# Kernel optimization log

Measured on AMD Instinct MI355X. Metric: run time of the kernel, lower is better.

## Reference

```python
import jax, jax.numpy as jnp
import numpy as np

N_NODES = 50000
N_EDGES = 1600000
HIDDEN = 64
N_BLOCKS = 2
N_ITERS = 2


def setup_inputs() -> dict:
    key = jax.random.key(0)
    ks = jax.random.split(key, 10)
    hidden = jax.random.normal(ks[0], (N_NODES, HIDDEN), dtype=jnp.float32)
    src = jax.random.randint(ks[1], (N_EDGES,), 0, N_NODES)
    dst = jax.random.randint(ks[2], (N_EDGES,), 0, N_NODES)
    s = 0.05  # keep MLP activations well-scaled
    W1 = jax.random.normal(ks[3], (N_BLOCKS, 3 * HIDDEN, 128), dtype=jnp.float32) * s
    b1 = jax.random.normal(ks[4], (N_BLOCKS, 128), dtype=jnp.float32) * s
    W2 = jax.random.normal(ks[5], (N_BLOCKS, 128, 128), dtype=jnp.float32) * s
    b2 = jax.random.normal(ks[6], (N_BLOCKS, 128), dtype=jnp.float32) * s
    W3 = jax.random.normal(ks[7], (N_BLOCKS, 128, HIDDEN), dtype=jnp.float32) * s
    b3 = jax.random.normal(ks[8], (N_BLOCKS, HIDDEN), dtype=jnp.float32) * s
    return {"hidden": hidden, "src": src, "dst": dst,
            "W1": W1, "b1": b1, "W2": W2, "b2": b2, "W3": W3, "b3": b3}


def _node_update(hidden, src, dst, w1, c1, w2, c2, w3, c3):
    # global rep: sum of all node hidden reps, broadcast to every node
    grep = jnp.broadcast_to(jnp.sum(hidden, axis=0, keepdims=True), hidden.shape)
    # mailbox sum: gather src features, segment-sum into dst
    msgs = hidden[src]                                  # [E, H]
    agg = jax.ops.segment_sum(msgs, dst, num_segments=hidden.shape[0])  # [N, H]
    x = jnp.concatenate([agg, hidden, grep], axis=1)    # [N, 3H]
    h = jax.nn.relu(x @ w1 + c1)
    h = jax.nn.relu(h @ w2 + c2)
    out = h @ w3 + c3
    # row-wise L2 (fro over dim=1) normalization
    norm = jnp.sqrt(jnp.sum(out * out, axis=1, keepdims=True))
    return out / norm


def reference(hidden, src, dst, W1, b1, W2, b2, W3, b3):
    for blk in range(N_BLOCKS):
        for _ in range(N_ITERS):
            hidden = _node_update(hidden, src, dst,
                                  W1[blk], b1[blk], W2[blk], b2[blk], W3[blk], b3[blk])
    return hidden
```

## Files before the change

kernel.cpp:

```cpp
#include <hip/hip_runtime.h>
#include <math.h>

#define NN 50000
#define NE 1600000
#define H  64

#define SHIFT 7
#define NPBKT 128
#define NB    391
#define CHUNK 4096
#define NCH   391

typedef __attribute__((ext_vector_type(8))) short s16v8;
typedef __attribute__((ext_vector_type(4))) float f32v4;
typedef __attribute__((ext_vector_type(8))) _Float16 f16v8;
typedef unsigned short u16;
typedef unsigned int   u32;

__device__ __forceinline__ u16 f2bf(float x) {
    union { float f; unsigned u; } v; v.f = x;
    unsigned r = v.u + 0x7FFF + ((v.u >> 16) & 1);
    return (u16)(r >> 16);
}
__device__ __forceinline__ float bf2f(u16 h) {
    union { float f; unsigned u; } v; v.u = ((unsigned)h) << 16; return v.f;
}

__global__ __launch_bounds__(256) void hist_kernel(const int* __restrict__ dst,
                                                   int* __restrict__ chunkhist) {
    __shared__ int h[NB];
    const int c = blockIdx.x;
    for (int b = threadIdx.x; b < NB; b += 256) h[b] = 0;
    __syncthreads();
    const int e0 = c * CHUNK, e1 = min(NE, e0 + CHUNK);
    for (int e = e0 + threadIdx.x; e < e1; e += 256)
        atomicAdd(&h[dst[e] >> SHIFT], 1);
    __syncthreads();
    for (int b = threadIdx.x; b < NB; b += 256)
        chunkhist[c * NB + b] = h[b];
}

__global__ __launch_bounds__(512) void cscan_kernel(int* __restrict__ chunkhist,
                                                    int* __restrict__ bbase) {
    __shared__ int s[512];
    const int t = threadIdx.x;
    int tot = 0;
    if (t < NB)
        for (int c = 0; c < NCH; ++c) tot += chunkhist[c * NB + t];
    s[t] = (t < NB) ? tot : 0;
    __syncthreads();
    for (int d = 1; d < 512; d <<= 1) {
        int v = (t >= d) ? s[t - d] : 0;
        __syncthreads();
        s[t] += v;
        __syncthreads();
    }
    if (t < NB) {
        int base = s[t] - tot;
        bbase[t] = base;
        if (t == NB - 1) bbase[NB] = s[t];
        int run = base;
        for (int c = 0; c < NCH; ++c) {
            int tmp = chunkhist[c * NB + t];
            chunkhist[c * NB + t] = run;
            run += tmp;
        }
    }
}

__global__ __launch_bounds__(256) void scat_kernel(const int* __restrict__ src,
                                                   const int* __restrict__ dst,
                                                   const int* __restrict__ chunkhist,
                                                   u32* __restrict__ bin) {
    __shared__ int base[NB];
    __shared__ int cur[NB];
    const int c = blockIdx.x;
    for (int b = threadIdx.x; b < NB; b += 256) {
        base[b] = chunkhist[c * NB + b];
        cur[b] = 0;
    }
    __syncthreads();
    const int e0 = c * CHUNK, e1 = min(NE, e0 + CHUNK);
    for (int e = e0 + threadIdx.x; e < e1; e += 256) {
        int d = dst[e];
        int b = d >> SHIFT;
        int p = atomicAdd(&cur[b], 1);
        bin[base[b] + p] = (u32)src[e] | ((u32)(d & (NPBKT - 1)) << 16);
    }
}

__global__ __launch_bounds__(256) void binB_kernel(const u32* __restrict__ bin,
                                                   const int* __restrict__ bbase,
                                                   int* __restrict__ off,
                                                   u16* __restrict__ csr) {
    __shared__ int deg[NPBKT];
    __shared__ int sc[NPBKT];
    __shared__ int cur[NPBKT];
    const int b = blockIdx.x, t = threadIdx.x;
    const int seg0 = bbase[b], seg1 = bbase[b + 1];
    if (t < NPBKT) { deg[t] = 0; cur[t] = 0; }
    __syncthreads();
    for (int i = seg0 + t; i < seg1; i += 256)
        atomicAdd(&deg[(bin[i] >> 16) & (NPBKT - 1)], 1);
    __syncthreads();
    if (t < NPBKT) sc[t] = deg[t];
    __syncthreads();
    for (int d = 1; d < NPBKT; d <<= 1) {
        int v = 0;
        if (t < NPBKT && t >= d) v = sc[t - d];
        __syncthreads();
        if (t < NPBKT) sc[t] += v;
        __syncthreads();
    }
    if (t < NPBKT) {
        sc[t] -= deg[t];
        int node = b * NPBKT + t;
        if (node < NN) off[node] = seg0 + sc[t];
        if (b == 0 && t == 0) off[NN] = NE;
    }
    __syncthreads();
    for (int i = seg0 + t; i < seg1; i += 256) {
        u32 e = bin[i];
        int n = (e >> 16) & (NPBKT - 1);
        int p = atomicAdd(&cur[n], 1);
        csr[seg0 + sc[n] + p] = (u16)(e & 0xFFFF);
    }
}

__global__ __launch_bounds__(256) void prep_kernel(const float* __restrict__ W1,
        const float* __restrict__ W2, const float* __restrict__ W3,
        u16* __restrict__ wt) {
    int idx = blockIdx.x * 256 + threadIdx.x;
    if (idx >= 2 * 40960) return;
    int b = idx / 40960, r = idx - b * 40960;
    float v; int hioff, losz;
    if (r < 16384) {
        int col = r >> 7, k = r & 127;
        v = W1[b * 24576 + k * 128 + col];
        hioff = b * 81920 + r; losz = 16384;
    } else if (r < 32768) {
        int rr = r - 16384; int col = rr >> 7, k = rr & 127;
        v = W2[b * 16384 + k * 128 + col];
        hioff = b * 81920 + 32768 + rr; losz = 16384;
    } else {
        int rr = r - 32768; int col = rr >> 7, k = rr & 127;
        v = W3[b * 8192 + k * 64 + col];
        hioff = b * 81920 + 65536 + rr; losz = 8192;
    }
    u16 hi = f2bf(v);
    u16 lo = f2bf(v - bf2f(hi));
    wt[hioff] = hi; wt[hioff + losz] = lo;
}

__global__ __launch_bounds__(256) void grep_kernel(const float* __restrict__ h,
                                                   float* __restrict__ partial,
                                                   _Float16* __restrict__ h16) {
    const int c  = threadIdx.x & 63;
    const int rl = threadIdx.x >> 6;
    float acc = 0.f;
    for (int r = blockIdx.x * 4 + rl; r < NN; r += gridDim.x * 4) {
        float v = h[r * H + c];
        h16[r * H + c] = (_Float16)v;
        acc += v;
    }
    __shared__ float s[4][64];
    s[rl][c] = acc;
    __syncthreads();
    if (threadIdx.x < 64)
        partial[blockIdx.x * 64 + threadIdx.x] =
            s[0][threadIdx.x] + s[1][threadIdx.x] +
            s[2][threadIdx.x] + s[3][threadIdx.x];
}

__global__ __launch_bounds__(1024) void b1e_kernel(const float* __restrict__ partial,
        int nparts,
        const float* __restrict__ W1, const float* __restrict__ b1,
        float* __restrict__ b1e) {
    __shared__ float sg[16][64];
    __shared__ float g[64];
    const int t = threadIdx.x;
    const int c = t & 63, rl = t >> 6;
    float s = 0.f;
    for (int i = rl; i < nparts; i += 16) s += partial[i * 64 + c];
    sg[rl][c] = s;
    __syncthreads();
    if (t < 64) {
        float a = 0.f;
#pragma unroll
        for (int j = 0; j < 16; ++j) a += sg[j][t];
        g[t] = a;
    }
    __syncthreads();
    if (t < 128) {
        float s2 = b1[t];
        for (int k = 0; k < 64; ++k)
            s2 = fmaf(g[k], W1[(128 + k) * 128 + t], s2);
        b1e[t] = s2;
    }
}

#define MLP_MFMA(d, a, b) d = __builtin_amdgcn_mfma_f32_16x16x32_bf16(a, b, d, 0, 0, 0)

__global__ __launch_bounds__(512, 4) void fused_mlp(
    const _Float16* __restrict__ h16in, const float* __restrict__ hin,
    const float* __restrict__ b1e, const u16* __restrict__ wt,
    const float* __restrict__ b2, const float* __restrict__ b3,
    const u16* __restrict__ csr, const int* __restrict__ off,
    float* __restrict__ out, _Float16* __restrict__ h16out,
    float* __restrict__ colpart)
{
    __shared__ u16 hhi[64 * 128], hlo[64 * 128];
    __shared__ float ssw[4][64];
    __shared__ float colp[64];
    const int t = threadIdx.x;
    const int wl = t >> 6, lane = t & 63;
    const int li = lane & 15, g = lane >> 4;
    const int n0 = blockIdx.x * 64;

    const u16* w1hi = wt;
    const u16* w1lo = wt + 16384;
    const u16* w2hi = wt + 32768;
    const u16* w2lo = wt + 49152;
    const u16* w3hi = wt + 65536;
    const u16* w3lo = wt + 73728;

    {
        const int nl = lane >> 3, sub = lane & 7;
        const int node = min(n0 + wl * 8 + nl, NN - 1);
        const int beg = off[node], end = off[node + 1];
        float a[8] = {0.f, 0.f, 0.f, 0.f, 0.f, 0.f, 0.f, 0.f};
        int e = beg;
        for (; e + 1 < end; e += 2) {
            const int s0 = csr[e], s1 = csr[e + 1];
            f16v8 v0 = *(const f16v8*)&h16in[(size_t)s0 * 64 + sub * 8];
            f16v8 v1 = *(const f16v8*)&h16in[(size_t)s1 * 64 + sub * 8];
#pragma unroll
            for (int j = 0; j < 8; ++j) a[j] += (float)v0[j] + (float)v1[j];
        }
        if (e < end) {
            const int s0 = csr[e];
            f16v8 v0 = *(const f16v8*)&h16in[(size_t)s0 * 64 + sub * 8];
#pragma unroll
            for (int j = 0; j < 8; ++j) a[j] += (float)v0[j];
        }
        const int row = wl * 8 + nl;
        s16v8 hv, lv;
#pragma unroll
        for (int j = 0; j < 8; ++j) {
            u16 hb = f2bf(a[j]);
            hv[j] = (short)hb;
            lv[j] = (short)f2bf(a[j] - bf2f(hb));
        }
        const int addr = row * 128 + ((sub ^ (row & 7)) << 3);
        *(s16v8*)&hhi[addr] = hv;
        *(s16v8*)&hlo[addr] = lv;
    }
    {
        const int row = t >> 3, c8 = t & 7;
        const int node = min(n0 + row, NN - 1);
        const float* sp = hin + (size_t)node * 64 + c8 * 8;
        float4 u0 = *(const float4*)sp;
        float4 u1 = *(const float4*)(sp + 4);
        float f[8] = {u0.x, u0.y, u0.z, u0.w, u1.x, u1.y, u1.z, u1.w};
        s16v8 hv, lv;
#pragma unroll
        for (int j = 0; j < 8; ++j) {
            u16 hb = f2bf(f[j]);
            hv[j] = (short)hb;
            lv[j] = (short)f2bf(f[j] - bf2f(hb));
        }
        const int cb = 8 + c8;
        const int addr = row * 128 + ((cb ^ (row & 7)) << 3);
        *(s16v8*)&hhi[addr] = hv;
        *(s16v8*)&hlo[addr] = lv;
    }
    __syncthreads();

    {
        const int col = wl * 16 + li;
        s16v8 Bh[4], Bl[4];
#pragma unroll
        for (int ks = 0; ks < 4; ++ks) {
            Bh[ks] = *(const s16v8*)(w1hi + col * 128 + ks * 32 + g * 8);
            Bl[ks] = *(const s16v8*)(w1lo + col * 128 + ks * 32 + g * 8);
        }
        f32v4 acc[4];
#pragma unroll
        for (int i = 0; i < 4; ++i) acc[i] = (f32v4){0.f, 0.f, 0.f, 0.f};
#pragma unroll
        for (int rt = 0; rt < 4; ++rt) {
            const int row = rt * 16 + li;
#pragma unroll
            for (int ks = 0; ks < 4; ++ks) {
                const int kb = ks * 4 + g;
                const int addr = row * 128 + ((kb ^ (row & 7)) << 3);
                s16v8 Ah = *(const s16v8*)&hhi[addr];
                s16v8 Al = *(const s16v8*)&hlo[addr];
                MLP_MFMA(acc[rt], Ah, Bh[ks]);
                MLP_MFMA(acc[rt], Ah, Bl[ks]);
                MLP_MFMA(acc[rt], Al, Bh[ks]);
            }
        }
        __syncthreads();
        const float bb = b1e[col];
        const int cb = col >> 3, c7 = col & 7;
#pragma unroll
        for (int rt = 0; rt < 4; ++rt) {
#pragma unroll
            for (int r = 0; r < 4; ++r) {
                float hv = fmaxf(acc[rt][r] + bb, 0.f);
                u16 hb = f2bf(hv);
                u16 lb = f2bf(hv - bf2f(hb));
                const int row = rt * 16 + g * 4 + r;
                const int addr = row * 128 + (((cb ^ (row & 7)) << 3) | c7);
                hhi[addr] = hb; hlo[addr] = lb;
            }
        }
    }
    __syncthreads();

    {
        const int col = wl * 16 + li;
        s16v8 Bh[4], Bl[4];
#pragma unroll
        for (int ks = 0; ks < 4; ++ks) {
            Bh[ks] = *(const s16v8*)(w2hi + col * 128 + ks * 32 + g * 8);
            Bl[ks] = *(const s16v8*)(w2lo + col * 128 + ks * 32 + g * 8);
        }
        f32v4 acc[4];
#pragma unroll
        for (int i = 0; i < 4; ++i) acc[i] = (f32v4){0.f, 0.f, 0.f, 0.f};
#pragma unroll
        for (int rt = 0; rt < 4; ++rt) {
            const int row = rt * 16 + li;
#pragma unroll
            for (int ks = 0; ks < 4; ++ks) {
                const int kb = ks * 4 + g;
                const int addr = row * 128 + ((kb ^ (row & 7)) << 3);
                s16v8 Ah = *(const s16v8*)&hhi[addr];
                s16v8 Al = *(const s16v8*)&hlo[addr];
                MLP_MFMA(acc[rt], Ah, Bh[ks]);
                MLP_MFMA(acc[rt], Ah, Bl[ks]);
                MLP_MFMA(acc[rt], Al, Bh[ks]);
            }
        }
        __syncthreads();
        const float bb = b2[col];
        const int cb = col >> 3, c7 = col & 7;
#pragma unroll
        for (int rt = 0; rt < 4; ++rt) {
#pragma unroll
            for (int r = 0; r < 4; ++r) {
                float hv = fmaxf(acc[rt][r] + bb, 0.f);
                u16 hb = f2bf(hv);
                u16 lb = f2bf(hv - bf2f(hb));
                const int row = rt * 16 + g * 4 + r;
                const int addr = row * 128 + (((cb ^ (row & 7)) << 3) | c7);
                hhi[addr] = hb; hlo[addr] = lb;
            }
        }
    }
    __syncthreads();

    float v[4][4];
    if (wl < 4) {
        const int col = wl * 16 + li;
        s16v8 Bh[4], Bl[4];
#pragma unroll
        for (int ks = 0; ks < 4; ++ks) {
            Bh[ks] = *(const s16v8*)(w3hi + col * 128 + ks * 32 + g * 8);
            Bl[ks] = *(const s16v8*)(w3lo + col * 128 + ks * 32 + g * 8);
        }
        f32v4 acc[4];
#pragma unroll
        for (int i = 0; i < 4; ++i) acc[i] = (f32v4){0.f, 0.f, 0.f, 0.f};
#pragma unroll
        for (int rt = 0; rt < 4; ++rt) {
            const int row = rt * 16 + li;
#pragma unroll
            for (int ks = 0; ks < 4; ++ks) {
                const int kb = ks * 4 + g;
                const int addr = row * 128 + ((kb ^ (row & 7)) << 3);
                s16v8 Ah = *(const s16v8*)&hhi[addr];
                s16v8 Al = *(const s16v8*)&hlo[addr];
                MLP_MFMA(acc[rt], Ah, Bh[ks]);
                MLP_MFMA(acc[rt], Ah, Bl[ks]);
                MLP_MFMA(acc[rt], Al, Bh[ks]);
            }
        }
        const float bb = b3[col];
#pragma unroll
        for (int rt = 0; rt < 4; ++rt) {
#pragma unroll
            for (int r = 0; r < 4; ++r) {
                float vv = acc[rt][r] + bb;
                v[rt][r] = vv;
                float s2 = vv * vv;
#pragma unroll
                for (int o = 1; o <= 8; o <<= 1) s2 += __shfl_xor(s2, o);
                if (li == 0) ssw[wl][rt * 16 + g * 4 + r] = s2;
            }
        }
    }
    __syncthreads();
    if (wl < 4) {
        const int col = wl * 16 + li;
        float cs = 0.f;
#pragma unroll
        for (int rt = 0; rt < 4; ++rt) {
#pragma unroll
            for (int r = 0; r < 4; ++r) {
                const int row = rt * 16 + g * 4 + r;
                const float tot = ssw[0][row] + ssw[1][row] +
                                  ssw[2][row] + ssw[3][row];
                const float inv = rsqrtf(tot);
                const int node = n0 + row;
                float ov = v[rt][r] * inv;
                if (node < NN) {
                    out[(size_t)node * 64 + col] = ov;
                    h16out[(size_t)node * 64 + col] = (_Float16)ov;
                    cs += ov;
                }
            }
        }
        cs += __shfl_xor(cs, 16);
        cs += __shfl_xor(cs, 32);
        if (g == 0) colp[col] = cs;
    }
    __syncthreads();
    if (t < 64)
        colpart[(size_t)blockIdx.x * 64 + t] = colp[t];
}

extern "C" void kernel_launch(void* const* d_in, const int* in_sizes, int n_in,
                              void* d_out, int out_size, void* d_ws, size_t ws_size,
                              hipStream_t stream) {
    const float* hidden = (const float*)d_in[0];
    const int*   src    = (const int*)d_in[1];
    const int*   dst    = (const int*)d_in[2];
    const float* W1f    = (const float*)d_in[3];
    const float* b1f    = (const float*)d_in[4];
    const float* W2f    = (const float*)d_in[5];
    const float* b2f    = (const float*)d_in[6];
    const float* W3f    = (const float*)d_in[7];
    const float* b3f    = (const float*)d_in[8];

    const int NBLK = (NN + 63) / 64;

    float* b1e     = (float*)d_ws;
    float* partA   = b1e + 128;
    float* partB   = partA + 256 * 64;
    float* hA      = partB + (size_t)NBLK * 64;
    int*   bbase   = (int*)(hA + (size_t)NN * H);
    int*   off     = bbase + (NB + 1);
    int*   chist   = off + (NN + 1);
    u32*   bin     = (u32*)(chist + NCH * NB);
    u16*   csr     = (u16*)(bin + NE);
    u16*   wt      = (u16*)(((uintptr_t)(csr + NE) + 255) & ~(uintptr_t)255);
    _Float16* h16a = (_Float16*)(wt + 2 * 81920);
    _Float16* h16b = h16a + (size_t)NN * H;

    hist_kernel<<<NCH, 256, 0, stream>>>(dst, chist);
    cscan_kernel<<<1, 512, 0, stream>>>(chist, bbase);
    scat_kernel<<<NCH, 256, 0, stream>>>(src, dst, chist, bin);
    binB_kernel<<<NB, 256, 0, stream>>>(bin, bbase, off, csr);
    prep_kernel<<<(2 * 40960 + 255) / 256, 256, 0, stream>>>(W1f, W2f, W3f, wt);

    grep_kernel<<<256, 256, 0, stream>>>(hidden, partA, h16a);

    const float* hin = hidden;
    float* houts[4] = { hA, (float*)d_out, hA, (float*)d_out };
    _Float16* h16bufs[2] = { h16a, h16b };

    for (int it = 0; it < 4; ++it) {
        const int blk = it >> 1;
        const float* part = (it == 0) ? partA : partB;
        const int nparts  = (it == 0) ? 256 : NBLK;
        b1e_kernel<<<1, 1024, 0, stream>>>(part, nparts,
            W1f + blk * 24576, b1f + blk * 128, b1e);
        fused_mlp<<<NBLK, 512, 0, stream>>>(
            h16bufs[it & 1], hin, b1e, wt + blk * 81920,
            b2f + blk * 128, b3f + blk * 64, csr, off,
            houts[it], h16bufs[(it + 1) & 1], partB);
        hin = houts[it];
    }
}
```

Measured before the change: 409.5 us.

## Fuse global-sum bias reduction into MLP kernel and unroll edge gather

Removes the separate single-block b1e kernel by having every fused_mlp block reduce the per-block column partials and compute the effective first-layer bias itself. Partial-sum buffers are ping-ponged so blocks can read the previous iteration's partials while writing new ones. The edge gather loop is unrolled to four edges and the self-feature load is issued earlier to overlap latency. This trades four small serial launches for redundant per-block reduction work over all partials.

```diff
diff --git a/kernel.cpp b/kernel.cpp
--- a/kernel.cpp
+++ b/kernel.cpp
@@ -172,38 +172,13 @@
             s[2][threadIdx.x] + s[3][threadIdx.x];
 }
 
-__global__ __launch_bounds__(1024) void b1e_kernel(const float* __restrict__ partial,
-        int nparts,
-        const float* __restrict__ W1, const float* __restrict__ b1,
-        float* __restrict__ b1e) {
-    __shared__ float sg[16][64];
-    __shared__ float g[64];
-    const int t = threadIdx.x;
-    const int c = t & 63, rl = t >> 6;
-    float s = 0.f;
-    for (int i = rl; i < nparts; i += 16) s += partial[i * 64 + c];
-    sg[rl][c] = s;
-    __syncthreads();
-    if (t < 64) {
-        float a = 0.f;
-#pragma unroll
-        for (int j = 0; j < 16; ++j) a += sg[j][t];
-        g[t] = a;
-    }
-    __syncthreads();
-    if (t < 128) {
-        float s2 = b1[t];
-        for (int k = 0; k < 64; ++k)
-            s2 = fmaf(g[k], W1[(128 + k) * 128 + t], s2);
-        b1e[t] = s2;
-    }
-}
-
 #define MLP_MFMA(d, a, b) d = __builtin_amdgcn_mfma_f32_16x16x32_bf16(a, b, d, 0, 0, 0)
 
 __global__ __launch_bounds__(512, 4) void fused_mlp(
     const _Float16* __restrict__ h16in, const float* __restrict__ hin,
-    const float* __restrict__ b1e, const u16* __restrict__ wt,
+    const float* __restrict__ part, int nparts,
+    const float* __restrict__ W1g, const float* __restrict__ b1,
+    const u16* __restrict__ wt,
     const float* __restrict__ b2, const float* __restrict__ b3,
     const u16* __restrict__ csr, const int* __restrict__ off,
     float* __restrict__ out, _Float16* __restrict__ h16out,
@@ -212,6 +187,8 @@
     __shared__ u16 hhi[64 * 128], hlo[64 * 128];
     __shared__ float ssw[4][64];
     __shared__ float colp[64];
+    __shared__ float gg[64];
+    __shared__ float b1eL[128];
     const int t = threadIdx.x;
     const int wl = t >> 6, lane = t & 63;
     const int li = lane & 15, g = lane >> 4;
@@ -225,54 +202,84 @@
     const u16* w3lo = wt + 73728;
 
     {
+        float* sgf = (float*)hhi;
+        const int c = t & 63, rl = t >> 6;
+        float s = 0.f;
+        for (int i = rl; i < nparts; i += 8) s += part[i * 64 + c];
+        sgf[rl * 64 + c] = s;
+        __syncthreads();
+        if (t < 64) {
+            float a = 0.f;
+#pragma unroll
+            for (int j = 0; j < 8; ++j) a += sgf[j * 64 + t];
+            gg[t] = a;
+        }
+        __syncthreads();
+        if (t < 128) {
+            float s2 = b1[t];
+            for (int k = 0; k < 64; ++k)
+                s2 = fmaf(gg[k], W1g[(128 + k) * 128 + t], s2);
+            b1eL[t] = s2;
+        }
+    }
+
+    {
+        const int row = t >> 3, c8 = t & 7;
+        const int hnode = min(n0 + row, NN - 1);
+        const float* sp = hin + (size_t)hnode * 64 + c8 * 8;
+        float4 u0 = *(const float4*)sp;
+        float4 u1 = *(const float4*)(sp + 4);
+
         const int nl = lane >> 3, sub = lane & 7;
         const int node = min(n0 + wl * 8 + nl, NN - 1);
         const int beg = off[node], end = off[node + 1];
         float a[8] = {0.f, 0.f, 0.f, 0.f, 0.f, 0.f, 0.f, 0.f};
         int e = beg;
-        for (; e + 1 < end; e += 2) {
-            const int s0 = csr[e], s1 = csr[e + 1];
+        for (; e + 3 < end; e += 4) {
+            const int s0 = csr[e],     s1 = csr[e + 1];
+            const int s2 = csr[e + 2], s3 = csr[e + 3];
             f16v8 v0 = *(const f16v8*)&h16in[(size_t)s0 * 64 + sub * 8];
             f16v8 v1 = *(const f16v8*)&h16in[(size_t)s1 * 64 + sub * 8];
-#pragma unroll
-            for (int j = 0; j < 8; ++j) a[j] += (float)v0[j] + (float)v1[j];
-        }
-        if (e < end) {
+            f16v8 v2 = *(const f16v8*)&h16in[(size_t)s2 * 64 + sub * 8];
+            f16v8 v3 = *(const f16v8*)&h16in[(size_t)s3 * 64 + sub * 8];
+#pragma unroll
+            for (int j = 0; j < 8; ++j)
+                a[j] += ((float)v0[j] + (float)v1[j]) +
+                        ((float)v2[j] + (float)v3[j]);
+        }
+        for (; e < end; ++e) {
             const int s0 = csr[e];
             f16v8 v0 = *(const f16v8*)&h16in[(size_t)s0 * 64 + sub * 8];
 #pragma unroll
             for (int j = 0; j < 8; ++j) a[j] += (float)v0[j];
         }
-        const int row = wl * 8 + nl;
-        s16v8 hv, lv;
-#pragma unroll
-        for (int j = 0; j < 8; ++j) {
-            u16 hb = f2bf(a[j]);
-            hv[j] = (short)hb;
-            lv[j] = (short)f2bf(a[j] - bf2f(hb));
-        }
-        const int addr = row * 128 + ((sub ^ (row & 7)) << 3);
-        *(s16v8*)&hhi[addr] = hv;
-        *(s16v8*)&hlo[addr] = lv;
-    }
-    {
-        const int row = t >> 3, c8 = t & 7;
-        const int node = min(n0 + row, NN - 1);
-        const float* sp = hin + (size_t)node * 64 + c8 * 8;
-        float4 u0 = *(const float4*)sp;
-        float4 u1 = *(const float4*)(sp + 4);
-        float f[8] = {u0.x, u0.y, u0.z, u0.w, u1.x, u1.y, u1.z, u1.w};
-        s16v8 hv, lv;
-#pragma unroll
-        for (int j = 0; j < 8; ++j) {
-            u16 hb = f2bf(f[j]);
-            hv[j] = (short)hb;
-            lv[j] = (short)f2bf(f[j] - bf2f(hb));
-        }
-        const int cb = 8 + c8;
-        const int addr = row * 128 + ((cb ^ (row & 7)) << 3);
-        *(s16v8*)&hhi[addr] = hv;
-        *(s16v8*)&hlo[addr] = lv;
+        {
+            const int grow = wl * 8 + nl;
+            s16v8 hv, lv;
+#pragma unroll
+            for (int j = 0; j < 8; ++j) {
+                u16 hb = f2bf(a[j]);
+                hv[j] = (short)hb;
+                lv[j] = (short)f2bf(a[j] - bf2f(hb));
+            }
+            const int addr = grow * 128 + ((sub ^ (grow & 7)) << 3);
+            *(s16v8*)&hhi[addr] = hv;
+            *(s16v8*)&hlo[addr] = lv;
+        }
+        {
+            float f[8] = {u0.x, u0.y, u0.z, u0.w, u1.x, u1.y, u1.z, u1.w};
+            s16v8 hv, lv;
+#pragma unroll
+            for (int j = 0; j < 8; ++j) {
+                u16 hb = f2bf(f[j]);
+                hv[j] = (short)hb;
+                lv[j] = (short)f2bf(f[j] - bf2f(hb));
+            }
+            const int cb = 8 + c8;
+            const int addr = row * 128 + ((cb ^ (row & 7)) << 3);
+            *(s16v8*)&hhi[addr] = hv;
+            *(s16v8*)&hlo[addr] = lv;
+        }
     }
     __syncthreads();
 
@@ -302,7 +309,7 @@
             }
         }
         __syncthreads();
-        const float bb = b1e[col];
+        const float bb = b1eL[col];
         const int cb = col >> 3, c7 = col & 7;
 #pragma unroll
         for (int rt = 0; rt < 4; ++rt) {
@@ -447,10 +454,10 @@
 
     const int NBLK = (NN + 63) / 64;
 
-    float* b1e     = (float*)d_ws;
-    float* partA   = b1e + 128;
+    float* partA   = (float*)d_ws;
     float* partB   = partA + 256 * 64;
-    float* hA      = partB + (size_t)NBLK * 64;
+    float* partC   = partB + (size_t)NBLK * 64;
+    float* hA      = partC + (size_t)NBLK * 64;
     int*   bbase   = (int*)(hA + (size_t)NN * H);
     int*   off     = bbase + (NB + 1);
     int*   chist   = off + (NN + 1);
@@ -471,17 +478,18 @@
     const float* hin = hidden;
     float* houts[4] = { hA, (float*)d_out, hA, (float*)d_out };
     _Float16* h16bufs[2] = { h16a, h16b };
+    const float* part_in[4]  = { partA, partB, partC, partB };
+    float*       part_out[4] = { partB, partC, partB, partC };
+    const int    nparts_in[4] = { 256, NBLK, NBLK, NBLK };
 
     for (int it = 0; it < 4; ++it) {
         const int blk = it >> 1;
-        const float* part = (it == 0) ? partA : partB;
-        const int nparts  = (it == 0) ? 256 : NBLK;
-        b1e_kernel<<<1, 1024, 0, stream>>>(part, nparts,
-            W1f + blk * 24576, b1f + blk * 128, b1e);
         fused_mlp<<<NBLK, 512, 0, stream>>>(
-            h16bufs[it & 1], hin, b1e, wt + blk * 81920,
-            b2f + blk * 128, b3f + blk * 64, csr, off,
-            houts[it], h16bufs[(it + 1) & 1], partB);
+            h16bufs[it & 1], hin, part_in[it], nparts_in[it],
+            W1f + blk * 24576, b1f + blk * 128,
+            wt + blk * 81920, b2f + blk * 128, b3f + blk * 64,
+            csr, off,
+            houts[it], h16bufs[(it + 1) & 1], part_out[it]);
         hin = houts[it];
     }
 }
```

Measured after the change: 487.8 us. 1.19x slower.

## Halve fused MLP node tile and widen neighbor gather to 16 lanes per node

Applied to the files above, without the earlier changes.

The fused MLP block now handles 32 nodes instead of 64, which doubles the grid and halves LDS use per block. The neighbor gather assigns 16 lanes per node with 4-element fp16 loads and unrolls by 4 edges, so more loads are in flight at once. Column partial sums now ping-pong between two buffers to fit the larger block count. The trade-off is that each block reloads the MLP weight fragments for half as many rows, and the MFMA work per weight load is smaller.

```diff
diff --git a/kernel.cpp b/kernel.cpp
--- a/kernel.cpp
+++ b/kernel.cpp
@@ -10,10 +10,12 @@
 #define NB    391
 #define CHUNK 4096
 #define NCH   391
+#define NBLK2 ((NN + 31) / 32)
 
 typedef __attribute__((ext_vector_type(8))) short s16v8;
+typedef __attribute__((ext_vector_type(4))) short s16v4;
 typedef __attribute__((ext_vector_type(4))) float f32v4;
-typedef __attribute__((ext_vector_type(8))) _Float16 f16v8;
+typedef __attribute__((ext_vector_type(4))) _Float16 f16v4;
 typedef unsigned short u16;
 typedef unsigned int   u32;
 
@@ -209,13 +211,13 @@
     float* __restrict__ out, _Float16* __restrict__ h16out,
     float* __restrict__ colpart)
 {
-    __shared__ u16 hhi[64 * 128], hlo[64 * 128];
-    __shared__ float ssw[4][64];
+    __shared__ u16 hhi[32 * 128], hlo[32 * 128];
+    __shared__ float ssw[4][32];
     __shared__ float colp[64];
     const int t = threadIdx.x;
     const int wl = t >> 6, lane = t & 63;
     const int li = lane & 15, g = lane >> 4;
-    const int n0 = blockIdx.x * 64;
+    const int n0 = blockIdx.x * 32;
 
     const u16* w1hi = wt;
     const u16* w1lo = wt + 16384;
@@ -225,54 +227,58 @@
     const u16* w3lo = wt + 73728;
 
     {
-        const int nl = lane >> 3, sub = lane & 7;
-        const int node = min(n0 + wl * 8 + nl, NN - 1);
+        const int row = t >> 4, sub = t & 15;
+        const int node = min(n0 + row, NN - 1);
         const int beg = off[node], end = off[node + 1];
-        float a[8] = {0.f, 0.f, 0.f, 0.f, 0.f, 0.f, 0.f, 0.f};
+        float a0 = 0.f, a1 = 0.f, a2 = 0.f, a3 = 0.f;
         int e = beg;
-        for (; e + 1 < end; e += 2) {
-            const int s0 = csr[e], s1 = csr[e + 1];
-            f16v8 v0 = *(const f16v8*)&h16in[(size_t)s0 * 64 + sub * 8];
-            f16v8 v1 = *(const f16v8*)&h16in[(size_t)s1 * 64 + sub * 8];
-#pragma unroll
-            for (int j = 0; j < 8; ++j) a[j] += (float)v0[j] + (float)v1[j];
-        }
-        if (e < end) {
+        for (; e + 3 < end; e += 4) {
+            const int s0 = csr[e],     s1 = csr[e + 1];
+            const int s2 = csr[e + 2], s3 = csr[e + 3];
+            f16v4 v0 = *(const f16v4*)&h16in[(size_t)s0 * 64 + sub * 4];
+            f16v4 v1 = *(const f16v4*)&h16in[(size_t)s1 * 64 + sub * 4];
+            f16v4 v2 = *(const f16v4*)&h16in[(size_t)s2 * 64 + sub * 4];
+            f16v4 v3 = *(const f16v4*)&h16in[(size_t)s3 * 64 + sub * 4];
+            a0 += ((float)v0[0] + (float)v1[0]) + ((float)v2[0] + (float)v3[0]);
+            a1 += ((float)v0[1] + (float)v1[1]) + ((float)v2[1] + (float)v3[1]);
+            a2 += ((float)v0[2] + (float)v1[2]) + ((float)v2[2] + (float)v3[2]);
+            a3 += ((float)v0[3] + (float)v1[3]) + ((float)v2[3] + (float)v3[3]);
+        }
+        for (; e < end; ++e) {
             const int s0 = csr[e];
-            f16v8 v0 = *(const f16v8*)&h16in[(size_t)s0 * 64 + sub * 8];
-#pragma unroll
-            for (int j = 0; j < 8; ++j) a[j] += (float)v0[j];
-        }
-        const int row = wl * 8 + nl;
-        s16v8 hv, lv;
-#pragma unroll
-        for (int j = 0; j < 8; ++j) {
-            u16 hb = f2bf(a[j]);
-            hv[j] = (short)hb;
-            lv[j] = (short)f2bf(a[j] - bf2f(hb));
-        }
-        const int addr = row * 128 + ((sub ^ (row & 7)) << 3);
-        *(s16v8*)&hhi[addr] = hv;
-        *(s16v8*)&hlo[addr] = lv;
-    }
-    {
-        const int row = t >> 3, c8 = t & 7;
-        const int node = min(n0 + row, NN - 1);
-        const float* sp = hin + (size_t)node * 64 + c8 * 8;
-        float4 u0 = *(const float4*)sp;
-        float4 u1 = *(const float4*)(sp + 4);
-        float f[8] = {u0.x, u0.y, u0.z, u0.w, u1.x, u1.y, u1.z, u1.w};
-        s16v8 hv, lv;
-#pragma unroll
-        for (int j = 0; j < 8; ++j) {
+            f16v4 v0 = *(const f16v4*)&h16in[(size_t)s0 * 64 + sub * 4];
+            a0 += (float)v0[0]; a1 += (float)v0[1];
+            a2 += (float)v0[2]; a3 += (float)v0[3];
+        }
+        float f[4] = {a0, a1, a2, a3};
+        s16v4 hv, lv;
+#pragma unroll
+        for (int j = 0; j < 4; ++j) {
             u16 hb = f2bf(f[j]);
             hv[j] = (short)hb;
             lv[j] = (short)f2bf(f[j] - bf2f(hb));
         }
-        const int cb = 8 + c8;
-        const int addr = row * 128 + ((cb ^ (row & 7)) << 3);
-        *(s16v8*)&hhi[addr] = hv;
-        *(s16v8*)&hlo[addr] = lv;
+        const int cb = sub >> 1, half = (sub & 1) * 4;
+        const int addr = row * 128 + (((cb ^ (row & 7)) << 3) | half);
+        *(s16v4*)&hhi[addr] = hv;
+        *(s16v4*)&hlo[addr] = lv;
+    }
+    {
+        const int row = t >> 4, c4 = t & 15;
+        const int node = min(n0 + row, NN - 1);
+        float4 u0 = *(const float4*)&hin[(size_t)node * 64 + c4 * 4];
+        float f[4] = {u0.x, u0.y, u0.z, u0.w};
+        s16v4 hv, lv;
+#pragma unroll
+        for (int j = 0; j < 4; ++j) {
+            u16 hb = f2bf(f[j]);
+            hv[j] = (short)hb;
+            lv[j] = (short)f2bf(f[j] - bf2f(hb));
+        }
+        const int cb = 8 + (c4 >> 1), half = (c4 & 1) * 4;
+        const int addr = row * 128 + (((cb ^ (row & 7)) << 3) | half);
+        *(s16v4*)&hhi[addr] = hv;
+        *(s16v4*)&hlo[addr] = lv;
     }
     __syncthreads();
 
@@ -284,11 +290,11 @@
             Bh[ks] = *(const s16v8*)(w1hi + col * 128 + ks * 32 + g * 8);
             Bl[ks] = *(const s16v8*)(w1lo + col * 128 + ks * 32 + g * 8);
         }
-        f32v4 acc[4];
-#pragma unroll
-        for (int i = 0; i < 4; ++i) acc[i] = (f32v4){0.f, 0.f, 0.f, 0.f};
-#pragma unroll
-        for (int rt = 0; rt < 4; ++rt) {
+        f32v4 acc[2];
+#pragma unroll
+        for (int i = 0; i < 2; ++i) acc[i] = (f32v4){0.f, 0.f, 0.f, 0.f};
+#pragma unroll
+        for (int rt = 0; rt < 2; ++rt) {
             const int row = rt * 16 + li;
 #pragma unroll
             for (int ks = 0; ks < 4; ++ks) {
@@ -305,7 +311,7 @@
         const float bb = b1e[col];
         const int cb = col >> 3, c7 = col & 7;
 #pragma unroll
-        for (int rt = 0; rt < 4; ++rt) {
+        for (int rt = 0; rt < 2; ++rt) {
 #pragma unroll
             for (int r = 0; r < 4; ++r) {
                 float hv = fmaxf(acc[rt][r] + bb, 0.f);
@@ -327,11 +333,11 @@
             Bh[ks] = *(const s16v8*)(w2hi + col * 128 + ks * 32 + g * 8);
             Bl[ks] = *(const s16v8*)(w2lo + col * 128 + ks * 32 + g * 8);
         }
-        f32v4 acc[4];
-#pragma unroll
-        for (int i = 0; i < 4; ++i) acc[i] = (f32v4){0.f, 0.f, 0.f, 0.f};
-#pragma unroll
-        for (int rt = 0; rt < 4; ++rt) {
+        f32v4 acc[2];
+#pragma unroll
+        for (int i = 0; i < 2; ++i) acc[i] = (f32v4){0.f, 0.f, 0.f, 0.f};
+#pragma unroll
+        for (int rt = 0; rt < 2; ++rt) {
             const int row = rt * 16 + li;
 #pragma unroll
             for (int ks = 0; ks < 4; ++ks) {
@@ -348,7 +354,7 @@
         const float bb = b2[col];
         const int cb = col >> 3, c7 = col & 7;
 #pragma unroll
-        for (int rt = 0; rt < 4; ++rt) {
+        for (int rt = 0; rt < 2; ++rt) {
 #pragma unroll
             for (int r = 0; r < 4; ++r) {
                 float hv = fmaxf(acc[rt][r] + bb, 0.f);
@@ -362,7 +368,7 @@
     }
     __syncthreads();
 
-    float v[4][4];
+    float v[2][4];
     if (wl < 4) {
         const int col = wl * 16 + li;
         s16v8 Bh[4], Bl[4];
@@ -371,11 +377,11 @@
             Bh[ks] = *(const s16v8*)(w3hi + col * 128 + ks * 32 + g * 8);
             Bl[ks] = *(const s16v8*)(w3lo + col * 128 + ks * 32 + g * 8);
         }
-        f32v4 acc[4];
-#pragma unroll
-        for (int i = 0; i < 4; ++i) acc[i] = (f32v4){0.f, 0.f, 0.f, 0.f};
-#pragma unroll
-        for (int rt = 0; rt < 4; ++rt) {
+        f32v4 acc[2];
+#pragma unroll
+        for (int i = 0; i < 2; ++i) acc[i] = (f32v4){0.f, 0.f, 0.f, 0.f};
+#pragma unroll
+        for (int rt = 0; rt < 2; ++rt) {
             const int row = rt * 16 + li;
 #pragma unroll
             for (int ks = 0; ks < 4; ++ks) {
@@ -390,7 +396,7 @@
         }
         const float bb = b3[col];
 #pragma unroll
-        for (int rt = 0; rt < 4; ++rt) {
+        for (int rt = 0; rt < 2; ++rt) {
 #pragma unroll
             for (int r = 0; r < 4; ++r) {
                 float vv = acc[rt][r] + bb;
@@ -407,7 +413,7 @@
         const int col = wl * 16 + li;
         float cs = 0.f;
 #pragma unroll
-        for (int rt = 0; rt < 4; ++rt) {
+        for (int rt = 0; rt < 2; ++rt) {
 #pragma unroll
             for (int r = 0; r < 4; ++r) {
                 const int row = rt * 16 + g * 4 + r;
@@ -445,12 +451,11 @@
     const float* W3f    = (const float*)d_in[7];
     const float* b3f    = (const float*)d_in[8];
 
-    const int NBLK = (NN + 63) / 64;
-
     float* b1e     = (float*)d_ws;
     float* partA   = b1e + 128;
     float* partB   = partA + 256 * 64;
-    float* hA      = partB + (size_t)NBLK * 64;
+    float* partC   = partB + (size_t)NBLK2 * 64;
+    float* hA      = partC + (size_t)NBLK2 * 64;
     int*   bbase   = (int*)(hA + (size_t)NN * H);
     int*   off     = bbase + (NB + 1);
     int*   chist   = off + (NN + 1);
@@ -471,17 +476,19 @@
     const float* hin = hidden;
     float* houts[4] = { hA, (float*)d_out, hA, (float*)d_out };
     _Float16* h16bufs[2] = { h16a, h16b };
+    const float* part_in[4]  = { partA, partB, partC, partB };
+    float*       part_out[4] = { partB, partC, partB, partC };
+    const int    nparts_in[4] = { 256, NBLK2, NBLK2, NBLK2 };
 
     for (int it = 0; it < 4; ++it) {
         const int blk = it >> 1;
-        const float* part = (it == 0) ? partA : partB;
-        const int nparts  = (it == 0) ? 256 : NBLK;
-        b1e_kernel<<<1, 1024, 0, stream>>>(part, nparts,
+        b1e_kernel<<<1, 1024, 0, stream>>>(part_in[it], nparts_in[it],
             W1f + blk * 24576, b1f + blk * 128, b1e);
-        fused_mlp<<<NBLK, 512, 0, stream>>>(
-            h16bufs[it & 1], hin, b1e, wt + blk * 81920,
-            b2f + blk * 128, b3f + blk * 64, csr, off,
-            houts[it], h16bufs[(it + 1) & 1], partB);
+        fused_mlp<<<NBLK2, 512, 0, stream>>>(
+            h16bufs[it & 1], hin, b1e,
+            wt + blk * 81920, b2f + blk * 128, b3f + blk * 64,
+            csr, off,
+            houts[it], h16bufs[(it + 1) & 1], part_out[it]);
         hin = houts[it];
     }
 }
```

Result: slower. 464.9 us (+13.5%).

## Balance neighbor aggregation across threads with edge-partitioned segmented reduction

Applied to the files above, without the earlier changes.

The CSR entries now pack the local destination index alongside the source, so each block splits its 64 nodes' edges evenly across all threads instead of giving each 8-lane group one node. Each thread walks contiguous edge runs, accumulates per destination, and flushes partial sums to a shared-memory fp32 accumulator with LDS atomics. The hin load is hoisted before the aggregation to overlap latency. This targets load imbalance from varying node degrees, at the cost of doubling CSR storage and bandwidth (u32 instead of u16) plus shared atomic traffic and extra barriers.

```diff
diff --git a/kernel.cpp b/kernel.cpp
--- a/kernel.cpp
+++ b/kernel.cpp
@@ -10,6 +10,7 @@
 #define NB    391
 #define CHUNK 4096
 #define NCH   391
+#define NBLK  ((NN + 63) / 64)
 
 typedef __attribute__((ext_vector_type(8))) short s16v8;
 typedef __attribute__((ext_vector_type(4))) float f32v4;
@@ -92,7 +93,7 @@
 __global__ __launch_bounds__(256) void binB_kernel(const u32* __restrict__ bin,
                                                    const int* __restrict__ bbase,
                                                    int* __restrict__ off,
-                                                   u16* __restrict__ csr) {
+                                                   u32* __restrict__ csr2) {
     __shared__ int deg[NPBKT];
     __shared__ int sc[NPBKT];
     __shared__ int cur[NPBKT];
@@ -123,7 +124,7 @@
         u32 e = bin[i];
         int n = (e >> 16) & (NPBKT - 1);
         int p = atomicAdd(&cur[n], 1);
-        csr[seg0 + sc[n] + p] = (u16)(e & 0xFFFF);
+        csr2[seg0 + sc[n] + p] = (e & 0xFFFF) | ((u32)n << 16);
     }
 }
 
@@ -205,7 +206,7 @@
     const _Float16* __restrict__ h16in, const float* __restrict__ hin,
     const float* __restrict__ b1e, const u16* __restrict__ wt,
     const float* __restrict__ b2, const float* __restrict__ b3,
-    const u16* __restrict__ csr, const int* __restrict__ off,
+    const u32* __restrict__ csr2, const int* __restrict__ off,
     float* __restrict__ out, _Float16* __restrict__ h16out,
     float* __restrict__ colpart)
 {
@@ -224,55 +225,97 @@
     const u16* w3hi = wt + 65536;
     const u16* w3lo = wt + 73728;
 
+    float* xaccf = (float*)hlo;
+
+#pragma unroll
+    for (int i = 0; i < 8; ++i) xaccf[i * 512 + t] = 0.f;
+    const int row_t = t >> 3, g8 = t & 7;
+    const int hnode = min(n0 + row_t, NN - 1);
+    float4 u0 = *(const float4*)(hin + (size_t)hnode * 64 + g8 * 8);
+    float4 u1 = *(const float4*)(hin + (size_t)hnode * 64 + g8 * 8 + 4);
+    __syncthreads();
+
     {
-        const int nl = lane >> 3, sub = lane & 7;
-        const int node = min(n0 + wl * 8 + nl, NN - 1);
-        const int beg = off[node], end = off[node + 1];
-        float a[8] = {0.f, 0.f, 0.f, 0.f, 0.f, 0.f, 0.f, 0.f};
-        int e = beg;
-        for (; e + 1 < end; e += 2) {
-            const int s0 = csr[e], s1 = csr[e + 1];
-            f16v8 v0 = *(const f16v8*)&h16in[(size_t)s0 * 64 + sub * 8];
-            f16v8 v1 = *(const f16v8*)&h16in[(size_t)s1 * 64 + sub * 8];
-#pragma unroll
-            for (int j = 0; j < 8; ++j) a[j] += (float)v0[j] + (float)v1[j];
-        }
-        if (e < end) {
-            const int s0 = csr[e];
-            f16v8 v0 = *(const f16v8*)&h16in[(size_t)s0 * 64 + sub * 8];
-#pragma unroll
-            for (int j = 0; j < 8; ++j) a[j] += (float)v0[j];
-        }
-        const int row = wl * 8 + nl;
+        const int E0 = off[n0];
+        const int E1 = off[min(n0 + 64, NN)];
+        const int E  = E1 - E0;
+        const int oct = t >> 3;
+        const int stripoff = n0 & 127;
+        const int per = (E + 255) >> 8;
+        int curn[4];
+        float a[4][8];
+#pragma unroll
+        for (int c = 0; c < 4; ++c) {
+            curn[c] = -1;
+#pragma unroll
+            for (int j = 0; j < 8; ++j) a[c][j] = 0.f;
+        }
+        for (int k = 0; k < per; ++k) {
+#pragma unroll
+            for (int c = 0; c < 4; ++c) {
+                const int cb = E0 + (oct * 4 + c) * per;
+                const int e = cb + k;
+                if (e < min(cb + per, E1)) {
+                    const u32 p = csr2[e];
+                    const int d = (int)(p >> 16) - stripoff;
+                    if (d != curn[c]) {
+                        if (curn[c] >= 0) {
+#pragma unroll
+                            for (int j = 0; j < 8; ++j)
+                                atomicAdd(&xaccf[curn[c] * 64 + g8 * 8 + j], a[c][j]);
+                        }
+                        curn[c] = d;
+#pragma unroll
+                        for (int j = 0; j < 8; ++j) a[c][j] = 0.f;
+                    }
+                    f16v8 v = *(const f16v8*)&h16in[(size_t)(p & 0xFFFFu) * 64 + g8 * 8];
+#pragma unroll
+                    for (int j = 0; j < 8; ++j) a[c][j] += (float)v[j];
+                }
+            }
+        }
+#pragma unroll
+        for (int c = 0; c < 4; ++c) {
+            if (curn[c] >= 0) {
+#pragma unroll
+                for (int j = 0; j < 8; ++j)
+                    atomicAdd(&xaccf[curn[c] * 64 + g8 * 8 + j], a[c][j]);
+            }
+        }
+    }
+    __syncthreads();
+
+    float xa[8];
+    {
+        const int base = row_t * 64 + g8 * 8;
+#pragma unroll
+        for (int j = 0; j < 8; ++j) xa[j] = xaccf[base + j];
+    }
+    __syncthreads();
+
+    {
         s16v8 hv, lv;
 #pragma unroll
         for (int j = 0; j < 8; ++j) {
-            u16 hb = f2bf(a[j]);
+            u16 hb = f2bf(xa[j]);
             hv[j] = (short)hb;
-            lv[j] = (short)f2bf(a[j] - bf2f(hb));
-        }
-        const int addr = row * 128 + ((sub ^ (row & 7)) << 3);
+            lv[j] = (short)f2bf(xa[j] - bf2f(hb));
+        }
+        const int addr = row_t * 128 + ((g8 ^ (row_t & 7)) << 3);
         *(s16v8*)&hhi[addr] = hv;
         *(s16v8*)&hlo[addr] = lv;
-    }
-    {
-        const int row = t >> 3, c8 = t & 7;
-        const int node = min(n0 + row, NN - 1);
-        const float* sp = hin + (size_t)node * 64 + c8 * 8;
-        float4 u0 = *(const float4*)sp;
-        float4 u1 = *(const float4*)(sp + 4);
         float f[8] = {u0.x, u0.y, u0.z, u0.w, u1.x, u1.y, u1.z, u1.w};
-        s16v8 hv, lv;
+        s16v8 hv2, lv2;
 #pragma unroll
         for (int j = 0; j < 8; ++j) {
             u16 hb = f2bf(f[j]);
-            hv[j] = (short)hb;
-            lv[j] = (short)f2bf(f[j] - bf2f(hb));
-        }
-        const int cb = 8 + c8;
-        const int addr = row * 128 + ((cb ^ (row & 7)) << 3);
-        *(s16v8*)&hhi[addr] = hv;
-        *(s16v8*)&hlo[addr] = lv;
+            hv2[j] = (short)hb;
+            lv2[j] = (short)f2bf(f[j] - bf2f(hb));
+        }
+        const int cb2 = 8 + g8;
+        const int addr2 = row_t * 128 + ((cb2 ^ (row_t & 7)) << 3);
+        *(s16v8*)&hhi[addr2] = hv2;
+        *(s16v8*)&hlo[addr2] = lv2;
     }
     __syncthreads();
 
@@ -445,8 +488,6 @@
     const float* W3f    = (const float*)d_in[7];
     const float* b3f    = (const float*)d_in[8];
 
-    const int NBLK = (NN + 63) / 64;
-
     float* b1e     = (float*)d_ws;
     float* partA   = b1e + 128;
     float* partB   = partA + 256 * 64;
@@ -455,15 +496,15 @@
     int*   off     = bbase + (NB + 1);
     int*   chist   = off + (NN + 1);
     u32*   bin     = (u32*)(chist + NCH * NB);
-    u16*   csr     = (u16*)(bin + NE);
-    u16*   wt      = (u16*)(((uintptr_t)(csr + NE) + 255) & ~(uintptr_t)255);
+    u32*   csr2    = bin + NE;
+    u16*   wt      = (u16*)(((uintptr_t)(csr2 + NE) + 255) & ~(uintptr_t)255);
     _Float16* h16a = (_Float16*)(wt + 2 * 81920);
     _Float16* h16b = h16a + (size_t)NN * H;
 
     hist_kernel<<<NCH, 256, 0, stream>>>(dst, chist);
     cscan_kernel<<<1, 512, 0, stream>>>(chist, bbase);
     scat_kernel<<<NCH, 256, 0, stream>>>(src, dst, chist, bin);
-    binB_kernel<<<NB, 256, 0, stream>>>(bin, bbase, off, csr);
+    binB_kernel<<<NB, 256, 0, stream>>>(bin, bbase, off, csr2);
     prep_kernel<<<(2 * 40960 + 255) / 256, 256, 0, stream>>>(W1f, W2f, W3f, wt);
 
     grep_kernel<<<256, 256, 0, stream>>>(hidden, partA, h16a);
@@ -479,8 +520,9 @@
         b1e_kernel<<<1, 1024, 0, stream>>>(part, nparts,
             W1f + blk * 24576, b1f + blk * 128, b1e);
         fused_mlp<<<NBLK, 512, 0, stream>>>(
-            h16bufs[it & 1], hin, b1e, wt + blk * 81920,
-            b2f + blk * 128, b3f + blk * 64, csr, off,
+            h16bufs[it & 1], hin, b1e,
+            wt + blk * 81920, b2f + blk * 128, b3f + blk * 64,
+            csr2, off,
             houts[it], h16bufs[(it + 1) & 1], partB);
         hin = houts[it];
     }
```

New measurement: 759.4 us. +85.5%, slower.
